# Performance work log

Measured on AMD Instinct MI355X. Metric: run time of the kernel, lower is better.

Reference implementation:

```python
import jax, jax.numpy as jnp
import numpy as np

SEQ, BATCH, IN, HID, OUT = 2048, 128, 256, 512, 256


def setup_inputs() -> dict:
    key = jax.random.key(0)
    ks = jax.random.split(key, 7)
    s_ih = 1.0 / np.sqrt(HID)
    return {
        "x": jax.random.normal(ks[0], (SEQ, BATCH, IN), dtype=jnp.float32),
        "W_ih": jax.random.normal(ks[1], (HID, IN), dtype=jnp.float32) * s_ih,
        "W_hh": jax.random.normal(ks[2], (HID, HID), dtype=jnp.float32) * s_ih,
        "b_ih": jax.random.normal(ks[3], (HID,), dtype=jnp.float32) * s_ih,
        "b_hh": jax.random.normal(ks[4], (HID,), dtype=jnp.float32) * s_ih,
        "W_fc": jax.random.normal(ks[5], (OUT, HID), dtype=jnp.float32) * s_ih,
        "b_fc": jax.random.normal(ks[6], (OUT,), dtype=jnp.float32) * s_ih,
    }


def reference(x, W_ih, W_hh, b_ih, b_hh, W_fc, b_fc):
    # Precompute input projections for all timesteps with one big GEMM:
    # [S, B, I] @ [I, H] -> [S, B, H]
    x_proj = jnp.einsum("sbi,hi->sbh", x, W_ih) + b_ih + b_hh

    def step(h, xp):  # h: [B, H], xp: [B, H]
        h_new = jnp.tanh(xp + h @ W_hh.T)
        return h_new, None

    h0 = jnp.zeros((x.shape[1], W_hh.shape[0]), dtype=x.dtype)
    h_last, _ = jax.lax.scan(step, h0, x_proj)
    # fc on last timestep's hidden state -> [B, OUT]
    return h_last @ W_fc.T + b_fc
```

## Files before the change

### kernel.cpp

```cpp
#include <hip/hip_runtime.h>
#include <stdint.h>

#define SEQ   2048
#define BATCH 128
#define DIN   256
#define DH    512
#define DOUT  256

typedef uint16_t u16;
typedef uint32_t u32;
typedef __attribute__((ext_vector_type(8))) short short8;
typedef __attribute__((ext_vector_type(4))) float f32x4;
typedef __attribute__((ext_vector_type(4))) int i32x4;

__device__ __forceinline__ u16 f2bf(float f) {
    u32 u = __float_as_uint(f);
    u += 0x7fffu + ((u >> 16) & 1u);
    return (u16)(u >> 16);
}
__device__ __forceinline__ float bf2f(u16 h) {
    return __uint_as_float(((u32)h) << 16);
}

__global__ __launch_bounds__(256) void wmax_kernel(const float* __restrict__ W,
                                                   unsigned* __restrict__ wmax) {
    __shared__ float red[256];
    int idx = blockIdx.x * 256 + threadIdx.x;
    float m = 0.f;
#pragma unroll
    for (int j = 0; j < 4; ++j) m = fmaxf(m, fabsf(W[(size_t)idx * 4 + j]));
    red[threadIdx.x] = m;
    __syncthreads();
    for (int s = 128; s > 0; s >>= 1) {
        if (threadIdx.x < s) red[threadIdx.x] = fmaxf(red[threadIdx.x], red[threadIdx.x + s]);
        __syncthreads();
    }
    if (threadIdx.x == 0) atomicMax(wmax, __float_as_uint(red[0]));
}

__global__ __launch_bounds__(256) void pack_whh_i8_kernel(
    const float* __restrict__ W, const unsigned* __restrict__ wmax,
    char* __restrict__ Wq) {
    int idx  = blockIdx.x * 256 + threadIdx.x;
    int lane = idx & 63;
    int n    = (idx >> 6) & 3;
    int kc   = (idx >> 8) & 7;
    int wv   = idx >> 11;
    float s = 127.0f / __uint_as_float(*wmax);
    int col = wv * 64 + n * 16 + (lane & 15);
    int k0  = kc * 64 + (lane >> 4) * 16;
    char q[16];
#pragma unroll
    for (int j = 0; j < 16; ++j)
        q[j] = (char)(int)rintf(W[(size_t)col * DH + k0 + j] * s);
    *reinterpret_cast<i32x4*>(Wq + (size_t)idx * 16) = *reinterpret_cast<i32x4*>(q);
}

__global__ __launch_bounds__(512) void xproj_kernel(
    const float* __restrict__ x, const float* __restrict__ W_ih,
    const float* __restrict__ b_ih, const float* __restrict__ b_hh,
    u16* __restrict__ xp) {
    __shared__ u16 As[128 * 64];
    __shared__ u16 Bs[256 * 64];
    const int tid  = threadIdx.x;
    const int lane = tid & 63;
    const int wid  = tid >> 6;
    const int wm   = wid >> 2;
    const int wn   = wid & 3;
    const int mt   = blockIdx.x;
    const int nt   = blockIdx.y;

    f32x4 acc[4][4];
#pragma unroll
    for (int i = 0; i < 4; ++i)
#pragma unroll
        for (int j = 0; j < 4; ++j) acc[i][j] = (f32x4){0.f, 0.f, 0.f, 0.f};

    for (int kk = 0; kk < DIN; kk += 64) {
        __syncthreads();
        {
            int r = tid >> 2, q = tid & 3;
            const float4* gp = (const float4*)(x + (size_t)(mt * 128 + r) * DIN + kk + q * 16);
            float4 v0 = gp[0], v1 = gp[1], v2 = gp[2], v3 = gp[3];
            short8 h0, h1;
            h0[0]=(short)f2bf(v0.x); h0[1]=(short)f2bf(v0.y); h0[2]=(short)f2bf(v0.z); h0[3]=(short)f2bf(v0.w);
            h0[4]=(short)f2bf(v1.x); h0[5]=(short)f2bf(v1.y); h0[6]=(short)f2bf(v1.z); h0[7]=(short)f2bf(v1.w);
            h1[0]=(short)f2bf(v2.x); h1[1]=(short)f2bf(v2.y); h1[2]=(short)f2bf(v2.z); h1[3]=(short)f2bf(v2.w);
            h1[4]=(short)f2bf(v3.x); h1[5]=(short)f2bf(v3.y); h1[6]=(short)f2bf(v3.z); h1[7]=(short)f2bf(v3.w);
            int base = r * 64, sw = (r & 7) << 3, ke = q * 16;
            *(short8*)&As[base + (ke ^ sw)]       = h0;
            *(short8*)&As[base + ((ke + 8) ^ sw)] = h1;
        }
        {
            int r = tid >> 1, hf = tid & 1;
            const float4* gp = (const float4*)(W_ih + (size_t)(nt * 256 + r) * DIN + kk + hf * 32);
            int base = r * 64, sw = (r & 7) << 3;
#pragma unroll
            for (int cp = 0; cp < 2; ++cp) {
                float4 u0 = gp[cp*4+0], u1 = gp[cp*4+1], u2 = gp[cp*4+2], u3 = gp[cp*4+3];
                short8 t0, t1;
                t0[0]=(short)f2bf(u0.x); t0[1]=(short)f2bf(u0.y); t0[2]=(short)f2bf(u0.z); t0[3]=(short)f2bf(u0.w);
                t0[4]=(short)f2bf(u1.x); t0[5]=(short)f2bf(u1.y); t0[6]=(short)f2bf(u1.z); t0[7]=(short)f2bf(u1.w);
                t1[0]=(short)f2bf(u2.x); t1[1]=(short)f2bf(u2.y); t1[2]=(short)f2bf(u2.z); t1[3]=(short)f2bf(u2.w);
                t1[4]=(short)f2bf(u3.x); t1[5]=(short)f2bf(u3.y); t1[6]=(short)f2bf(u3.z); t1[7]=(short)f2bf(u3.w);
                int ke = hf * 32 + cp * 16;
                *(short8*)&Bs[base + (ke ^ sw)]       = t0;
                *(short8*)&Bs[base + ((ke + 8) ^ sw)] = t1;
            }
        }
        __syncthreads();
#pragma unroll
        for (int kt = 0; kt < 2; ++kt) {
            short8 a[4], b[4];
            int ke = kt * 32 + (lane >> 4) * 8;
#pragma unroll
            for (int mi = 0; mi < 4; ++mi) {
                int rr = wm * 64 + mi * 16 + (lane & 15);
                a[mi] = *(const short8*)&As[rr * 64 + (ke ^ ((rr & 7) << 3))];
            }
#pragma unroll
            for (int ni = 0; ni < 4; ++ni) {
                int rr = wn * 64 + ni * 16 + (lane & 15);
                b[ni] = *(const short8*)&Bs[rr * 64 + (ke ^ ((rr & 7) << 3))];
            }
#pragma unroll
            for (int mi = 0; mi < 4; ++mi)
#pragma unroll
                for (int ni = 0; ni < 4; ++ni)
                    acc[mi][ni] = __builtin_amdgcn_mfma_f32_16x16x32_bf16(b[ni], a[mi], acc[mi][ni], 0, 0, 0);
        }
    }
    const int lq = lane >> 4;
#pragma unroll
    for (int ni = 0; ni < 4; ++ni) {
        int col0 = nt * 256 + wn * 64 + ni * 16 + lq * 4;
        float4 bi = *(const float4*)(b_ih + col0);
        float4 bh = *(const float4*)(b_hh + col0);
        float bb0 = bi.x + bh.x, bb1 = bi.y + bh.y, bb2 = bi.z + bh.z, bb3 = bi.w + bh.w;
#pragma unroll
        for (int mi = 0; mi < 4; ++mi) {
            float v0 = (acc[mi][ni][0] + bb0) * 2.0f;
            float v1 = (acc[mi][ni][1] + bb1) * 2.0f;
            float v2 = (acc[mi][ni][2] + bb2) * 2.0f;
            float v3 = (acc[mi][ni][3] + bb3) * 2.0f;
            uint2 v;
            v.x = (u32)f2bf(v0) | ((u32)f2bf(v1) << 16);
            v.y = (u32)f2bf(v2) | ((u32)f2bf(v3) << 16);
            int bbk = wm * 4 + mi;
            int cidx = (nt * 4 + wn) * 4 + ni;
            *(uint2*)(xp + ((((size_t)mt * 8 + bbk) * 32 + cidx) * 64 + lane) * 4) = v;
        }
    }
}

__global__ __launch_bounds__(512) void rnn_rec_kernel(
    const u16* __restrict__ xp, const char* __restrict__ Wq,
    const unsigned* __restrict__ wmax_p, u16* __restrict__ h_last) {
    __shared__ char h_s[2][16 * 512];
    const int tid = threadIdx.x, lane = tid & 63, wv = tid >> 6;
    const int bg = blockIdx.x;
    const int row = lane & 15, lq = lane >> 4;
    const int sw = (row & 7) << 4;
    const float sc2 = __uint_as_float(*wmax_p) * (2.0f / (127.f * 127.f));

    i32x4 wrr[8][4];
#pragma unroll
    for (int kc = 0; kc < 8; ++kc)
#pragma unroll
        for (int n = 0; n < 4; ++n) {
            wrr[kc][n] = *(const i32x4*)(Wq + (size_t)((wv * 8 + kc) * 4 + n) * 1024 + lane * 16);
            asm volatile("" : "+v"(wrr[kc][n]));
        }

    *(i32x4*)&h_s[0][tid * 32]      = (i32x4){0, 0, 0, 0};
    *(i32x4*)&h_s[0][tid * 32 + 16] = (i32x4){0, 0, 0, 0};

    const u16* xpp = xp + (((size_t)(bg * 32 + wv * 4) * 64) + lane) * 4;
    uint2 xn[4];
#pragma unroll
    for (int n = 0; n < 4; ++n) xn[n] = *(const uint2*)(xpp + n * 256);
    xpp += 65536;

    __syncthreads();

    for (int t = 0; t < SEQ; ++t) {
        const int cur = t & 1, nxt = cur ^ 1;

        uint2 xc[4];
#pragma unroll
        for (int n = 0; n < 4; ++n) xc[n] = xn[n];
        if (t + 1 < SEQ) {
#pragma unroll
            for (int n = 0; n < 4; ++n) xn[n] = *(const uint2*)(xpp + n * 256);
            xpp += 65536;
        }

        i32x4 acc[4];
#pragma unroll
        for (int n = 0; n < 4; ++n) acc[n] = (i32x4){0, 0, 0, 0};

#pragma unroll
        for (int kc = 0; kc < 8; ++kc) {
            i32x4 hf = *(const i32x4*)&h_s[cur][row * 512 + ((kc * 64 + lq * 16) ^ sw)];
#pragma unroll
            for (int n = 0; n < 4; ++n)
                acc[n] = __builtin_amdgcn_mfma_i32_16x16x64_i8(wrr[kc][n], hf, acc[n], 0, 0, 0);
        }

#pragma unroll
        for (int n = 0; n < 4; ++n) {
            float t0 = fmaf((float)acc[n][0], sc2, __uint_as_float(xc[n].x << 16));
            float t1 = fmaf((float)acc[n][1], sc2, __uint_as_float(xc[n].x & 0xffff0000u));
            float t2 = fmaf((float)acc[n][2], sc2, __uint_as_float(xc[n].y << 16));
            float t3 = fmaf((float)acc[n][3], sc2, __uint_as_float(xc[n].y & 0xffff0000u));
            float r0 = __builtin_amdgcn_rcpf(__expf(t0) + 1.0f);
            float r1 = __builtin_amdgcn_rcpf(__expf(t1) + 1.0f);
            float r2 = __builtin_amdgcn_rcpf(__expf(t2) + 1.0f);
            float r3 = __builtin_amdgcn_rcpf(__expf(t3) + 1.0f);
            int colb = wv * 64 + n * 16 + lq * 4;
            if (t == SEQ - 1) {
                float h0 = fmaf(-2.f, r0, 1.f), h1 = fmaf(-2.f, r1, 1.f);
                float h2 = fmaf(-2.f, r2, 1.f), h3 = fmaf(-2.f, r3, 1.f);
                uint2 hv;
                hv.x = (u32)f2bf(h0) | ((u32)f2bf(h1) << 16);
                hv.y = (u32)f2bf(h2) | ((u32)f2bf(h3) << 16);
                *(uint2*)(h_last + (size_t)(bg * 16 + row) * DH + colb) = hv;
            } else {
                u32 b0 = __float_as_uint(fmaf(-254.f, r0, 12583039.f));
                u32 b1 = __float_as_uint(fmaf(-254.f, r1, 12583039.f));
                u32 b2 = __float_as_uint(fmaf(-254.f, r2, 12583039.f));
                u32 b3 = __float_as_uint(fmaf(-254.f, r3, 12583039.f));
                u32 p01 = __builtin_amdgcn_perm(b1, b0, 0x00000400u);
                u32 p23 = __builtin_amdgcn_perm(b3, b2, 0x00000400u);
                u32 pk  = __builtin_amdgcn_perm(p23, p01, 0x05040100u);
                *(u32*)&h_s[nxt][row * 512 + (colb ^ sw)] = pk;
            }
        }
        if (t == SEQ - 1) break;
        __syncthreads();
    }
}

__global__ __launch_bounds__(256) void fc_kernel(
    const u16* __restrict__ h_last, const float* __restrict__ W_fc,
    const float* __restrict__ b_fc, float* __restrict__ out) {
    __shared__ float hsh[DH];
    int b = blockIdx.x, o = threadIdx.x;
    for (int i = threadIdx.x; i < DH; i += 256) hsh[i] = bf2f(h_last[(size_t)b * DH + i]);
    __syncthreads();
    const float* w = W_fc + (size_t)o * DH;
    float s = 0.f;
#pragma unroll 8
    for (int k = 0; k < DH; ++k) s += hsh[k] * w[k];
    out[(size_t)b * DOUT + o] = s + b_fc[o];
}

extern "C" void kernel_launch(void* const* d_in, const int* in_sizes, int n_in,
                              void* d_out, int out_size, void* d_ws, size_t ws_size,
                              hipStream_t stream) {
    const float* x    = (const float*)d_in[0];
    const float* W_ih = (const float*)d_in[1];
    const float* W_hh = (const float*)d_in[2];
    const float* b_ih = (const float*)d_in[3];
    const float* b_hh = (const float*)d_in[4];
    const float* W_fc = (const float*)d_in[5];
    const float* b_fc = (const float*)d_in[6];
    float* out = (float*)d_out;

    char* base    = (char*)d_ws;
    u16*  xp      = (u16*)base;
    char* Wq      = base + (size_t)SEQ * BATCH * DH * 2;
    u16*  h_last  = (u16*)(Wq + (size_t)DH * DH);
    unsigned* wmx = (unsigned*)((char*)h_last + (size_t)BATCH * DH * 2);

    hipMemsetAsync(wmx, 0, sizeof(unsigned), stream);
    hipLaunchKernelGGL(wmax_kernel, dim3(256), dim3(256), 0, stream, W_hh, wmx);
    hipLaunchKernelGGL(pack_whh_i8_kernel, dim3(64), dim3(256), 0, stream, W_hh, wmx, Wq);
    hipLaunchKernelGGL(xproj_kernel, dim3(2048, 2), dim3(512), 0, stream, x, W_ih, b_ih, b_hh, xp);
    hipLaunchKernelGGL(rnn_rec_kernel, dim3(8), dim3(512), 0, stream, xp, Wq, wmx, h_last);
    hipLaunchKernelGGL(fc_kernel, dim3(128), dim3(256), 0, stream, h_last, W_fc, b_fc, out);
}
```

Baseline: 2.825 ms.

## Split recurrent step across 16 waves per block and fold log2e into exponent

Doubles the recurrent kernel's block size from 8 to 16 waves, so each wave owns 32 hidden columns (two MFMA tiles) instead of 64. This halves the serial MFMA chain and the register-resident weights per wave, aiming to shorten the per-timestep critical path. The weight packing layout changes to match. It also pre-scales the input projection and the recurrent scale by 2*log2(e) so the kernel can use exp2f directly and skip the ln2 multiply. A large dummy shared-memory pad is added, presumably to force one block per CU. The risks are heavier barrier synchronisation across more waves per step and extra LDS traffic for the h broadcast.

```diff
diff --git a/kernel.cpp b/kernel.cpp
--- a/kernel.cpp
+++ b/kernel.cpp
@@ -13,6 +13,8 @@
 typedef __attribute__((ext_vector_type(4))) float f32x4;
 typedef __attribute__((ext_vector_type(4))) int i32x4;
 
+#define TWO_LOG2E 2.8853900817779268f
+
 __device__ __forceinline__ u16 f2bf(float f) {
     u32 u = __float_as_uint(f);
     u += 0x7fffu + ((u >> 16) & 1u);
@@ -43,16 +45,15 @@
     char* __restrict__ Wq) {
     int idx  = blockIdx.x * 256 + threadIdx.x;
     int lane = idx & 63;
-    int n    = (idx >> 6) & 3;
-    int kc   = (idx >> 8) & 7;
-    int wv   = idx >> 11;
-    float s = 127.0f / __uint_as_float(*wmax);
-    int col = wv * 64 + n * 16 + (lane & 15);
+    int kc   = (idx >> 6) & 7;
+    int s    = idx >> 9;
+    float sc = 127.0f / __uint_as_float(*wmax);
+    int col = s * 16 + (lane & 15);
     int k0  = kc * 64 + (lane >> 4) * 16;
     char q[16];
 #pragma unroll
     for (int j = 0; j < 16; ++j)
-        q[j] = (char)(int)rintf(W[(size_t)col * DH + k0 + j] * s);
+        q[j] = (char)(int)rintf(W[(size_t)col * DH + k0 + j] * sc);
     *reinterpret_cast<i32x4*>(Wq + (size_t)idx * 16) = *reinterpret_cast<i32x4*>(q);
 }
 
@@ -139,10 +140,10 @@
         float bb0 = bi.x + bh.x, bb1 = bi.y + bh.y, bb2 = bi.z + bh.z, bb3 = bi.w + bh.w;
 #pragma unroll
         for (int mi = 0; mi < 4; ++mi) {
-            float v0 = (acc[mi][ni][0] + bb0) * 2.0f;
-            float v1 = (acc[mi][ni][1] + bb1) * 2.0f;
-            float v2 = (acc[mi][ni][2] + bb2) * 2.0f;
-            float v3 = (acc[mi][ni][3] + bb3) * 2.0f;
+            float v0 = (acc[mi][ni][0] + bb0) * TWO_LOG2E;
+            float v1 = (acc[mi][ni][1] + bb1) * TWO_LOG2E;
+            float v2 = (acc[mi][ni][2] + bb2) * TWO_LOG2E;
+            float v3 = (acc[mi][ni][3] + bb3) * TWO_LOG2E;
             uint2 v;
             v.x = (u32)f2bf(v0) | ((u32)f2bf(v1) << 16);
             v.y = (u32)f2bf(v2) | ((u32)f2bf(v3) << 16);
@@ -153,32 +154,34 @@
     }
 }
 
-__global__ __launch_bounds__(512) void rnn_rec_kernel(
+__global__ __launch_bounds__(1024) void rnn_rec_kernel(
     const u16* __restrict__ xp, const char* __restrict__ Wq,
     const unsigned* __restrict__ wmax_p, u16* __restrict__ h_last) {
     __shared__ char h_s[2][16 * 512];
+    __shared__ char occ_pad[81920];
     const int tid = threadIdx.x, lane = tid & 63, wv = tid >> 6;
     const int bg = blockIdx.x;
     const int row = lane & 15, lq = lane >> 4;
     const int sw = (row & 7) << 4;
-    const float sc2 = __uint_as_float(*wmax_p) * (2.0f / (127.f * 127.f));
-
-    i32x4 wrr[8][4];
+    const float sc2 = __uint_as_float(*wmax_p) * (TWO_LOG2E / (127.f * 127.f));
+
+    if (blockIdx.x >= 1000) occ_pad[tid] = 0;
+
+    i32x4 wrr[8][2];
 #pragma unroll
     for (int kc = 0; kc < 8; ++kc)
 #pragma unroll
-        for (int n = 0; n < 4; ++n) {
-            wrr[kc][n] = *(const i32x4*)(Wq + (size_t)((wv * 8 + kc) * 4 + n) * 1024 + lane * 16);
+        for (int n = 0; n < 2; ++n) {
+            wrr[kc][n] = *(const i32x4*)(Wq + (size_t)((wv * 2 + n) * 8 + kc) * 1024 + lane * 16);
             asm volatile("" : "+v"(wrr[kc][n]));
         }
 
-    *(i32x4*)&h_s[0][tid * 32]      = (i32x4){0, 0, 0, 0};
-    *(i32x4*)&h_s[0][tid * 32 + 16] = (i32x4){0, 0, 0, 0};
-
-    const u16* xpp = xp + (((size_t)(bg * 32 + wv * 4) * 64) + lane) * 4;
-    uint2 xn[4];
-#pragma unroll
-    for (int n = 0; n < 4; ++n) xn[n] = *(const uint2*)(xpp + n * 256);
+    *(i32x4*)&h_s[0][tid * 16] = (i32x4){0, 0, 0, 0};
+
+    const u16* xpp = xp + (((size_t)(bg * 32 + wv * 2) * 64) + lane) * 4;
+    uint2 xn[2];
+#pragma unroll
+    for (int n = 0; n < 2; ++n) xn[n] = *(const uint2*)(xpp + n * 256);
     xpp += 65536;
 
     __syncthreads();
@@ -186,38 +189,37 @@
     for (int t = 0; t < SEQ; ++t) {
         const int cur = t & 1, nxt = cur ^ 1;
 
-        uint2 xc[4];
-#pragma unroll
-        for (int n = 0; n < 4; ++n) xc[n] = xn[n];
+        uint2 xc[2];
+#pragma unroll
+        for (int n = 0; n < 2; ++n) xc[n] = xn[n];
         if (t + 1 < SEQ) {
 #pragma unroll
-            for (int n = 0; n < 4; ++n) xn[n] = *(const uint2*)(xpp + n * 256);
+            for (int n = 0; n < 2; ++n) xn[n] = *(const uint2*)(xpp + n * 256);
             xpp += 65536;
         }
 
-        i32x4 acc[4];
-#pragma unroll
-        for (int n = 0; n < 4; ++n) acc[n] = (i32x4){0, 0, 0, 0};
+        i32x4 acc[2];
+        acc[0] = (i32x4){0, 0, 0, 0};
+        acc[1] = (i32x4){0, 0, 0, 0};
 
 #pragma unroll
         for (int kc = 0; kc < 8; ++kc) {
             i32x4 hf = *(const i32x4*)&h_s[cur][row * 512 + ((kc * 64 + lq * 16) ^ sw)];
-#pragma unroll
-            for (int n = 0; n < 4; ++n)
-                acc[n] = __builtin_amdgcn_mfma_i32_16x16x64_i8(wrr[kc][n], hf, acc[n], 0, 0, 0);
-        }
-
-#pragma unroll
-        for (int n = 0; n < 4; ++n) {
+            acc[0] = __builtin_amdgcn_mfma_i32_16x16x64_i8(wrr[kc][0], hf, acc[0], 0, 0, 0);
+            acc[1] = __builtin_amdgcn_mfma_i32_16x16x64_i8(wrr[kc][1], hf, acc[1], 0, 0, 0);
+        }
+
+#pragma unroll
+        for (int n = 0; n < 2; ++n) {
             float t0 = fmaf((float)acc[n][0], sc2, __uint_as_float(xc[n].x << 16));
             float t1 = fmaf((float)acc[n][1], sc2, __uint_as_float(xc[n].x & 0xffff0000u));
             float t2 = fmaf((float)acc[n][2], sc2, __uint_as_float(xc[n].y << 16));
             float t3 = fmaf((float)acc[n][3], sc2, __uint_as_float(xc[n].y & 0xffff0000u));
-            float r0 = __builtin_amdgcn_rcpf(__expf(t0) + 1.0f);
-            float r1 = __builtin_amdgcn_rcpf(__expf(t1) + 1.0f);
-            float r2 = __builtin_amdgcn_rcpf(__expf(t2) + 1.0f);
-            float r3 = __builtin_amdgcn_rcpf(__expf(t3) + 1.0f);
-            int colb = wv * 64 + n * 16 + lq * 4;
+            float r0 = __builtin_amdgcn_rcpf(exp2f(t0) + 1.0f);
+            float r1 = __builtin_amdgcn_rcpf(exp2f(t1) + 1.0f);
+            float r2 = __builtin_amdgcn_rcpf(exp2f(t2) + 1.0f);
+            float r3 = __builtin_amdgcn_rcpf(exp2f(t3) + 1.0f);
+            int colb = wv * 32 + n * 16 + lq * 4;
             if (t == SEQ - 1) {
                 float h0 = fmaf(-2.f, r0, 1.f), h1 = fmaf(-2.f, r1, 1.f);
                 float h2 = fmaf(-2.f, r2, 1.f), h3 = fmaf(-2.f, r3, 1.f);
@@ -277,6 +279,6 @@
     hipLaunchKernelGGL(wmax_kernel, dim3(256), dim3(256), 0, stream, W_hh, wmx);
     hipLaunchKernelGGL(pack_whh_i8_kernel, dim3(64), dim3(256), 0, stream, W_hh, wmx, Wq);
     hipLaunchKernelGGL(xproj_kernel, dim3(2048, 2), dim3(512), 0, stream, x, W_ih, b_ih, b_hh, xp);
-    hipLaunchKernelGGL(rnn_rec_kernel, dim3(8), dim3(512), 0, stream, xp, Wq, wmx, h_last);
+    hipLaunchKernelGGL(rnn_rec_kernel, dim3(8), dim3(1024), 0, stream, xp, Wq, wmx, h_last);
     hipLaunchKernelGGL(fc_kernel, dim3(128), dim3(256), 0, stream, h_last, W_fc, b_fc, out);
 }
```

Result: slower. 2.928 ms (+3.7%).
